# Kernel tuning notes

Hardware: AMD Instinct MI355X
Metric: run time of the kernel (lower is better)

The kernel has to match this reference:

```python
import jax, jax.numpy as jnp
import numpy as np

B, T, D, H = 2, 2048, 1024, 16
HD = D // H  # 64


def setup_inputs() -> dict:
    key = jax.random.key(0)
    ks = jax.random.split(key, 9)
    w = lambda k, shp: (jax.random.normal(k, shp, jnp.float32) * 0.02)
    return {
        "x": jax.random.normal(ks[0], (B, T, D), jnp.float32),
        "Wq": w(ks[1], (D, D)), "bq": jnp.zeros((D,), jnp.float32),
        "Wk": w(ks[2], (D, D)), "bk": jnp.zeros((D,), jnp.float32),
        "Wv": w(ks[3], (D, D)), "bv": jnp.zeros((D,), jnp.float32),
        "Wo": w(ks[4], (D, D)), "bo": jnp.zeros((D,), jnp.float32),
        "Wqs": w(ks[5], (3, HD)), "bqs": jnp.zeros((3,), jnp.float32),
        "Wks": w(ks[6], (3, HD)), "bks": jnp.zeros((3,), jnp.float32),
        "Wvs": w(ks[7], (3, HD)), "bvs": jnp.zeros((3,), jnp.float32),
        "temp": jnp.float32(1.0),
    }


def reference(x, Wq, bq, Wk, bk, Wv, bv, Wo, bo, Wqs, bqs, Wks, bks, Wvs, bvs, temp):
    Bx, Tx, Dx = x.shape
    # project and split heads: [B,H,T,HD]
    split = lambda y: y.reshape(Bx, Tx, H, HD).transpose(0, 2, 1, 3)
    q = split(x @ Wq.T + bq)
    k = split(x @ Wk.T + bk)
    v = split(x @ Wv.T + bv)
    # STP projections to 3-d: [B,H,T,3]
    q_stp = q @ Wqs.T + bqs
    k3 = k @ Wks.T + bks
    v3 = v @ Wvs.T + bvs
    # cross-product term (note: original's layernormed k_sub/v_sub are dead code)
    cross_kv = jnp.cross(k3, v3, axis=-1)  # [B,H,T,3]
    scores = (jnp.einsum('bhqd,bhkd->bhqk', q, k)
              + jnp.einsum('bhqc,bhkc->bhqk', q_stp, cross_kv)) * temp
    attn = jax.nn.softmax(scores, axis=-1)
    out = jnp.einsum('bhqk,bhkd->bhqd', attn, v)  # [B,H,T,HD]
    out = out.transpose(0, 2, 1, 3).reshape(Bx, Tx, Dx)
    return out @ Wo.T + bo
```

## Files before the change

kernel.cpp:

```cpp
#include <hip/hip_runtime.h>
#include <stdint.h>

typedef unsigned short u16;
typedef unsigned int u32;
typedef __attribute__((ext_vector_type(8))) short bf16x8;
typedef __attribute__((ext_vector_type(4))) float f32x4;

__device__ __forceinline__ u16 f2b(float f) {
    union { float f; u32 u; } t; t.f = f;
    return (u16)((t.u + 0x7FFFu + ((t.u >> 16) & 1u)) >> 16);
}
__device__ __forceinline__ u32 pack2(float a, float b) {
    return (u32)f2b(a) | ((u32)f2b(b) << 16);
}
__device__ __forceinline__ u32 cvtpk2(float lo, float hi) {
    u32 r;
    asm("v_cvt_pk_bf16_f32 %0, %1, %2" : "=v"(r) : "v"(lo), "v"(hi));
    return r;
}

__device__ __forceinline__ void async_cp16(const u16* g, const u16* lds_base) {
    __builtin_amdgcn_global_load_lds(
        (const __attribute__((address_space(1))) void*)(uintptr_t)g,
        (__attribute__((address_space(3))) void*)(u32)(uintptr_t)lds_base,
        16, 0, 0);
}

__global__ void cast_all_kernel(const float* __restrict__ x,
                                const float* __restrict__ Wq, const float* __restrict__ Wk,
                                const float* __restrict__ Wv, const float* __restrict__ Wo,
                                u16* __restrict__ xb, u16* __restrict__ Wqb, u16* __restrict__ Wkb,
                                u16* __restrict__ Wvb, u16* __restrict__ Wob) {
    int i = blockIdx.x * blockDim.x + threadIdx.x;
    const float* s; u16* d; int off;
    if (i < 1048576) { s = x; d = xb; off = i; }
    else {
        int j = i - 1048576;
        int w = j >> 18; off = j & 262143;
        if (w == 0) { s = Wq; d = Wqb; }
        else if (w == 1) { s = Wk; d = Wkb; }
        else if (w == 2) { s = Wv; d = Wvb; }
        else { s = Wo; d = Wob; }
    }
    float4 f = ((const float4*)s)[off];
    ((uint2*)d)[off] = make_uint2(pack2(f.x, f.y), pack2(f.z, f.w));
}

__global__ __launch_bounds__(256) void gemm_qkv_kernel(
    const u16* __restrict__ xb,
    const u16* __restrict__ Wq, const u16* __restrict__ Wk, const u16* __restrict__ Wv,
    const float* __restrict__ bq, const float* __restrict__ bk, const float* __restrict__ bv,
    const float* __restrict__ Wqs, const float* __restrict__ bqs,
    const float* __restrict__ Wks, const float* __restrict__ bks,
    const float* __restrict__ Wvs, const float* __restrict__ bvs,
    const float* __restrict__ temp_p,
    u16* __restrict__ qe, u16* __restrict__ ke, u16* __restrict__ vT,
    float4* __restrict__ k3b, float4* __restrict__ v3b)
{
    __shared__ __align__(16) u16 As[2 * 64 * 32];
    __shared__ __align__(16) u16 Bs[2 * 128 * 32];
    const int tid = threadIdx.x;
    const int lane = tid & 63, w = tid >> 6;
    const int wm = w >> 1, wn = w & 1;
    const int l15 = lane & 15, quad = lane >> 4;
    const int M0 = blockIdx.y * 64, N0 = blockIdx.x * 128;
    const int bz = blockIdx.z;

    const u16* W = (bz == 0) ? Wq : (bz == 1) ? Wk : Wv;
    const float* bias = (bz == 0) ? bq : (bz == 1) ? bk : bv;
    const float* Wst = (bz == 0) ? Wqs : (bz == 1) ? Wks : Wvs;
    const float* bst = (bz == 0) ? bqs : (bz == 1) ? bks : bvs;

    f32x4 acc[2][4];
#pragma unroll
    for (int i = 0; i < 2; i++)
#pragma unroll
        for (int j = 0; j < 4; j++) acc[i][j] = (f32x4){0.f, 0.f, 0.f, 0.f};

    int ra = tid >> 2, ca = ((tid & 3) ^ (ra & 3)) * 8;
    const u16* Aga = xb + (size_t)(M0 + ra) * 1024 + ca;
    const u16* Bg0 = W + (size_t)(N0 + ra) * 1024 + ca;
    const u16* Bg1 = W + (size_t)(N0 + ra + 64) * 1024 + ca;
    const int aoff = (w * 64) * 8;
    const int boff0 = (w * 64) * 8;
    const int boff1 = (256 + w * 64) * 8;

    async_cp16(Aga, As + aoff);
    async_cp16(Bg0, Bs + boff0);
    async_cp16(Bg1, Bs + boff1);
    __syncthreads();

    for (int k0 = 0; k0 < 1024; k0 += 32) {
        const int buf = (k0 >> 5) & 1;
        const u16* Asr = As + buf * 2048;
        const u16* Bsr = Bs + buf * 4096;
        if (k0 + 32 < 1024) {
            const int nb_ = buf ^ 1;
            async_cp16(Aga + k0 + 32, As + nb_ * 2048 + aoff);
            async_cp16(Bg0 + k0 + 32, Bs + nb_ * 4096 + boff0);
            async_cp16(Bg1 + k0 + 32, Bs + nb_ * 4096 + boff1);
        }

        bf16x8 af[2], bf[4];
#pragma unroll
        for (int mi = 0; mi < 2; mi++)
            af[mi] = *(const bf16x8*)(Asr + (wm * 32 + mi * 16 + l15) * 32 + ((quad ^ (l15 & 3)) * 8));
#pragma unroll
        for (int ni = 0; ni < 4; ni++)
            bf[ni] = *(const bf16x8*)(Bsr + (wn * 64 + ni * 16 + l15) * 32 + ((quad ^ (l15 & 3)) * 8));
#pragma unroll
        for (int mi = 0; mi < 2; mi++)
#pragma unroll
            for (int ni = 0; ni < 4; ni++)
                acc[mi][ni] = __builtin_amdgcn_mfma_f32_16x16x32_bf16(af[mi], bf[ni], acc[mi][ni], 0, 0, 0);

        __syncthreads();
    }

    const float tau = temp_p[0] * 1.44269504088896f;
    const int nb = N0 + wn * 64;
    const int h = nb >> 6;
    float bias_v[4], wst_v[3][4];
#pragma unroll
    for (int ni = 0; ni < 4; ni++) {
        bias_v[ni] = bias[nb + ni * 16 + l15];
#pragma unroll
        for (int c = 0; c < 3; c++) wst_v[c][ni] = Wst[c * 64 + ni * 16 + l15];
    }
    const float bst0 = bst[0], bst1 = bst[1], bst2 = bst[2];

#pragma unroll
    for (int mi = 0; mi < 2; mi++) {
        int m0 = M0 + wm * 32 + mi * 16 + quad * 4;
        int b = m0 >> 11, t0 = m0 & 2047;
        float p0[4], p1[4], p2[4];
#pragma unroll
        for (int r = 0; r < 4; r++) {
            float a0 = 0.f, a1 = 0.f, a2 = 0.f;
#pragma unroll
            for (int ni = 0; ni < 4; ni++) {
                float v = acc[mi][ni][r] + bias_v[ni];
                a0 += v * wst_v[0][ni];
                a1 += v * wst_v[1][ni];
                a2 += v * wst_v[2][ni];
            }
#pragma unroll
            for (int off = 1; off < 16; off <<= 1) {
                a0 += __shfl_xor(a0, off);
                a1 += __shfl_xor(a1, off);
                a2 += __shfl_xor(a2, off);
            }
            p0[r] = a0 + bst0; p1[r] = a1 + bst1; p2[r] = a2 + bst2;
        }

        if (bz == 0) {
#pragma unroll
            for (int r = 0; r < 4; r++) {
                size_t row = (size_t)((b * 16 + h) * 2048 + (t0 + r));
                u16* qer = qe + row * 96;
#pragma unroll
                for (int ni = 0; ni < 4; ni++)
                    qer[ni * 16 + l15] = f2b((acc[mi][ni][r] + bias_v[ni]) * tau);
                if (l15 == 0) {
                    *(u32*)(qer + 64) = pack2(p0[r] * tau, p1[r] * tau);
                    *(u32*)(qer + 66) = (u32)f2b(p2[r] * tau);
                    uint2 z = make_uint2(0u, 0u);
#pragma unroll
                    for (int j = 68; j < 96; j += 4) *(uint2*)(qer + j) = z;
                }
            }
        } else if (bz == 1) {
#pragma unroll
            for (int r = 0; r < 4; r++) {
                size_t row = (size_t)((b * 16 + h) * 2048 + (t0 + r));
                u16* ker = ke + row * 96;
#pragma unroll
                for (int ni = 0; ni < 4; ni++)
                    ker[ni * 16 + l15] = f2b(acc[mi][ni][r] + bias_v[ni]);
                if (l15 == 0)
                    k3b[row] = make_float4(p0[r], p1[r], p2[r], 0.f);
            }
        } else {
#pragma unroll
            for (int ni = 0; ni < 4; ni++) {
                int hd = ni * 16 + l15;
                float v0 = acc[mi][ni][0] + bias_v[ni];
                float v1 = acc[mi][ni][1] + bias_v[ni];
                float v2 = acc[mi][ni][2] + bias_v[ni];
                float v3 = acc[mi][ni][3] + bias_v[ni];
                *(uint2*)(vT + ((size_t)((b * 16 + h) * 64 + hd)) * 2048 + t0) =
                    make_uint2(pack2(v0, v1), pack2(v2, v3));
            }
            if (l15 == 0) {
#pragma unroll
                for (int r = 0; r < 4; r++) {
                    size_t row = (size_t)((b * 16 + h) * 2048 + (t0 + r));
                    v3b[row] = make_float4(p0[r], p1[r], p2[r], 0.f);
                }
            }
        }
    }
}

__global__ void finish_ext_kernel(const float4* __restrict__ k3b, const float4* __restrict__ v3b,
                                  u16* __restrict__ ke)
{
    int row = blockIdx.x * blockDim.x + threadIdx.x;
    if (row >= 2 * 16 * 2048) return;
    float4 k3 = k3b[row];
    float4 v3 = v3b[row];
    float c0 = k3.y * v3.z - k3.z * v3.y;
    float c1 = k3.z * v3.x - k3.x * v3.z;
    float c2 = k3.x * v3.y - k3.y * v3.x;
    u16* ker = ke + (size_t)row * 96;
    *(u32*)(ker + 64) = pack2(c0, c1);
    *(u32*)(ker + 66) = (u32)f2b(c2);
    uint2 z = make_uint2(0u, 0u);
#pragma unroll
    for (int j = 68; j < 96; j += 4) *(uint2*)(ker + j) = z;
}

__global__ __launch_bounds__(256) void gemm_out_kernel(
    const u16* __restrict__ ao, const u16* __restrict__ Wo, const float* __restrict__ bo,
    float* __restrict__ out)
{
    __shared__ __align__(16) u16 As[2 * 64 * 32];
    __shared__ __align__(16) u16 Bs[2 * 128 * 32];
    const int tid = threadIdx.x;
    const int lane = tid & 63, w = tid >> 6;
    const int wm = w >> 1, wn = w & 1;
    const int l15 = lane & 15, quad = lane >> 4;
    const int M0 = blockIdx.y * 64, N0 = blockIdx.x * 128;

    f32x4 acc[2][4];
#pragma unroll
    for (int i = 0; i < 2; i++)
#pragma unroll
        for (int j = 0; j < 4; j++) acc[i][j] = (f32x4){0.f, 0.f, 0.f, 0.f};

    int ra = tid >> 2, ca = ((tid & 3) ^ (ra & 3)) * 8;
    const u16* Aga = ao + (size_t)(M0 + ra) * 1024 + ca;
    const u16* Bg0 = Wo + (size_t)(N0 + ra) * 1024 + ca;
    const u16* Bg1 = Wo + (size_t)(N0 + ra + 64) * 1024 + ca;
    const int aoff = (w * 64) * 8;
    const int boff0 = (w * 64) * 8;
    const int boff1 = (256 + w * 64) * 8;

    async_cp16(Aga, As + aoff);
    async_cp16(Bg0, Bs + boff0);
    async_cp16(Bg1, Bs + boff1);
    __syncthreads();

    for (int k0 = 0; k0 < 1024; k0 += 32) {
        const int buf = (k0 >> 5) & 1;
        const u16* Asr = As + buf * 2048;
        const u16* Bsr = Bs + buf * 4096;
        if (k0 + 32 < 1024) {
            const int nb_ = buf ^ 1;
            async_cp16(Aga + k0 + 32, As + nb_ * 2048 + aoff);
            async_cp16(Bg0 + k0 + 32, Bs + nb_ * 4096 + boff0);
            async_cp16(Bg1 + k0 + 32, Bs + nb_ * 4096 + boff1);
        }

        bf16x8 af[2], bf[4];
#pragma unroll
        for (int mi = 0; mi < 2; mi++)
            af[mi] = *(const bf16x8*)(Asr + (wm * 32 + mi * 16 + l15) * 32 + ((quad ^ (l15 & 3)) * 8));
#pragma unroll
        for (int ni = 0; ni < 4; ni++)
            bf[ni] = *(const bf16x8*)(Bsr + (wn * 64 + ni * 16 + l15) * 32 + ((quad ^ (l15 & 3)) * 8));
#pragma unroll
        for (int mi = 0; mi < 2; mi++)
#pragma unroll
            for (int ni = 0; ni < 4; ni++)
                acc[mi][ni] = __builtin_amdgcn_mfma_f32_16x16x32_bf16(af[mi], bf[ni], acc[mi][ni], 0, 0, 0);

        __syncthreads();
    }

#pragma unroll
    for (int mi = 0; mi < 2; mi++)
#pragma unroll
        for (int ni = 0; ni < 4; ni++) {
            int n = N0 + wn * 64 + ni * 16 + l15;
            float bias_n = bo[n];
            int m0 = M0 + wm * 32 + mi * 16 + quad * 4;
#pragma unroll
            for (int r = 0; r < 4; r++)
                out[(size_t)(m0 + r) * 1024 + n] = acc[mi][ni][r] + bias_n;
        }
}

__global__ __launch_bounds__(256, 2) void attn_kernel(
    const u16* __restrict__ qe, const u16* __restrict__ ke, const u16* __restrict__ vT,
    u16* __restrict__ out)
{
    __shared__ __align__(16) u16 smem[32768];
    u16* const KsA = smem;
    u16* const VtA = smem + 16384;
    u16* const PsB = smem + 24576;

    const int tid = threadIdx.x;
    const int lane = tid & 63, w = tid >> 6;
    const int kw = w & 1, qw = w >> 1;
    const int l15 = lane & 15, quad = lane >> 4;
    const int lsw = l15 & 7;
    const int bh = blockIdx.y;
    const int q0 = blockIdx.x * 128;

    const u16* qeb = qe + (size_t)bh * 2048 * 96;
    const u16* keb = ke + (size_t)bh * 2048 * 96;
    const u16* vTb = vT + (size_t)bh * 64 * 2048;

    size_t koff[4];
#pragma unroll
    for (int j = 0; j < 4; j++) {
        int r = w * 16 + j * 4 + (lane >> 4);
        koff[j] = (size_t)r * 96 + (size_t)((((lane & 15) ^ (r & 7)) * 8));
    }
    size_t voff[2];
#pragma unroll
    for (int j = 0; j < 2; j++) {
        int r = w * 16 + j * 8 + (lane >> 3);
        voff[j] = (size_t)r * 2048 + (size_t)((((lane & 7) ^ (r & 7)) * 8));
    }

#pragma unroll
    for (int j = 0; j < 4; j++) async_cp16(keb + koff[j], KsA + w * 2048 + j * 512);
#pragma unroll
    for (int j = 0; j < 2; j++) async_cp16(vTb + voff[j], VtA + w * 1024 + j * 512);

    bf16x8 bq[4][3];
#pragma unroll
    for (int s = 0; s < 4; s++) {
        const u16* qrow = qeb + (size_t)(q0 + qw * 64 + s * 16 + l15) * 96;
#pragma unroll
        for (int ks = 0; ks < 3; ks++) bq[s][ks] = *(const bf16x8*)(qrow + ks * 32 + quad * 8);
    }

    f32x4 O[4][4];
    float l_part[4];
#pragma unroll
    for (int s = 0; s < 4; s++) {
        l_part[s] = 0.f;
#pragma unroll
        for (int dt = 0; dt < 4; dt++) O[s][dt] = (f32x4){0.f, 0.f, 0.f, 0.f};
    }

    u16* Pw[4];
#pragma unroll
    for (int s = 0; s < 4; s++) Pw[s] = PsB + (size_t)(qw * 64 + s * 16 + l15) * 64;

    __syncthreads();

    for (int kb = 0; kb < 2048; kb += 64) {
        const int buf = (kb >> 6) & 1;
        const u16* Ks = KsA + buf * 8192;
        const u16* Vt = VtA + buf * 4096;

        if (kb + 64 < 2048) {
            u16* Ksn = KsA + (buf ^ 1) * 8192;
            u16* Vtn = VtA + (buf ^ 1) * 4096;
            const size_t kb96 = (size_t)(kb + 64) * 96;
#pragma unroll
            for (int j = 0; j < 4; j++) async_cp16(keb + kb96 + koff[j], Ksn + w * 2048 + j * 512);
#pragma unroll
            for (int j = 0; j < 2; j++) async_cp16(vTb + (size_t)(kb + 64) + voff[j], Vtn + w * 1024 + j * 512);
        }

        f32x4 S[4][2];
#pragma unroll
        for (int s = 0; s < 4; s++)
#pragma unroll
            for (int nt = 0; nt < 2; nt++) S[s][nt] = (f32x4){0.f, 0.f, 0.f, 0.f};

        __builtin_amdgcn_s_setprio(1);
#pragma unroll
        for (int ks = 0; ks < 3; ks++) {
            bf16x8 ak[2];
#pragma unroll
            for (int nt = 0; nt < 2; nt++)
                ak[nt] = *(const bf16x8*)(Ks + (kw * 32 + nt * 16 + l15) * 128 + (((ks * 4 + quad) ^ lsw) & 15) * 8);
#pragma unroll
            for (int s = 0; s < 4; s++)
#pragma unroll
                for (int nt = 0; nt < 2; nt++)
                    S[s][nt] = __builtin_amdgcn_mfma_f32_16x16x32_bf16(ak[nt], bq[s][ks], S[s][nt], 0, 0, 0);
        }
        __builtin_amdgcn_s_setprio(0);

#pragma unroll
        for (int s = 0; s < 4; s++) {
            float sum = 0.f;
#pragma unroll
            for (int nt = 0; nt < 2; nt++)
#pragma unroll
                for (int r = 0; r < 4; r++) {
                    float p = __builtin_amdgcn_exp2f(S[s][nt][r]);
                    S[s][nt][r] = p;
                    sum += p;
                }
            l_part[s] += sum;
#pragma unroll
            for (int nt = 0; nt < 2; nt++) {
                int c = (kw * 4 + nt * 2 + (quad >> 1)) ^ lsw;
                *(uint2*)(Pw[s] + c * 8 + (quad & 1) * 4) =
                    make_uint2(cvtpk2(S[s][nt][0], S[s][nt][1]), cvtpk2(S[s][nt][2], S[s][nt][3]));
            }
        }

        {
            bf16x8 av[4];
#pragma unroll
            for (int dt = 0; dt < 4; dt++)
                av[dt] = *(const bf16x8*)(Vt + (dt * 16 + l15) * 64 + (((kw * 4 + quad) ^ lsw) & 7) * 8);
            __builtin_amdgcn_s_setprio(1);
#pragma unroll
            for (int s = 0; s < 4; s++) {
                bf16x8 pb = *(const bf16x8*)(Pw[s] + (((kw * 4 + quad) ^ lsw) & 7) * 8);
#pragma unroll
                for (int dt = 0; dt < 4; dt++)
                    O[s][dt] = __builtin_amdgcn_mfma_f32_16x16x32_bf16(av[dt], pb, O[s][dt], 0, 0, 0);
            }
            __builtin_amdgcn_s_setprio(0);
        }

        __syncthreads();
    }

    float* const Ored = (float*)smem;
    float* const Lr = (float*)(smem + 20480);
    if (kw == 1) {
#pragma unroll
        for (int s = 0; s < 4; s++) {
            float l = l_part[s];
            l += __shfl_xor(l, 16);
            l += __shfl_xor(l, 32);
            if (lane < 16) Lr[qw * 64 + s * 16 + l15] = l;
            int qrow = qw * 64 + s * 16 + l15;
#pragma unroll
            for (int dt = 0; dt < 4; dt++) {
                int dc = dt ^ (l15 & 3);
                *(float4*)(Ored + qrow * 68 + dc * 16 + quad * 4) =
                    make_float4(O[s][dt][0], O[s][dt][1], O[s][dt][2], O[s][dt][3]);
            }
        }
    }
    __syncthreads();
    if (kw == 0) {
        const int b = bh >> 4, h = bh & 15;
#pragma unroll
        for (int s = 0; s < 4; s++) {
            float l = l_part[s];
            l += __shfl_xor(l, 16);
            l += __shfl_xor(l, 32);
            int qrow = qw * 64 + s * 16 + l15;
            l += Lr[qrow];
            float linv = 1.0f / l;
            int tq = q0 + qrow;
#pragma unroll
            for (int dt = 0; dt < 4; dt++) {
                int dc = dt ^ (l15 & 3);
                float4 o2 = *(const float4*)(Ored + qrow * 68 + dc * 16 + quad * 4);
                int d = h * 64 + dt * 16 + quad * 4;
                *(uint2*)(out + (size_t)(b * 2048 + tq) * 1024 + d) =
                    make_uint2(cvtpk2((O[s][dt][0] + o2.x) * linv, (O[s][dt][1] + o2.y) * linv),
                               cvtpk2((O[s][dt][2] + o2.z) * linv, (O[s][dt][3] + o2.w) * linv));
            }
        }
    }
}

extern "C" void kernel_launch(void* const* d_in, const int* in_sizes, int n_in,
                              void* d_out, int out_size, void* d_ws, size_t ws_size,
                              hipStream_t stream)
{
    (void)in_sizes; (void)n_in; (void)out_size; (void)ws_size;
    const float* x   = (const float*)d_in[0];
    const float* Wq  = (const float*)d_in[1];
    const float* bq  = (const float*)d_in[2];
    const float* Wk  = (const float*)d_in[3];
    const float* bk  = (const float*)d_in[4];
    const float* Wv  = (const float*)d_in[5];
    const float* bv  = (const float*)d_in[6];
    const float* Wo  = (const float*)d_in[7];
    const float* bo  = (const float*)d_in[8];
    const float* Wqs = (const float*)d_in[9];
    const float* bqs = (const float*)d_in[10];
    const float* Wks = (const float*)d_in[11];
    const float* bks = (const float*)d_in[12];
    const float* Wvs = (const float*)d_in[13];
    const float* bvs = (const float*)d_in[14];
    const float* temp = (const float*)d_in[15];

    char* ws = (char*)d_ws;
    u16* xb  = (u16*)(ws);
    u16* Wqb = (u16*)(ws + 8388608);
    u16* Wkb = (u16*)(ws + 10485760);
    u16* Wvb = (u16*)(ws + 12582912);
    u16* Wob = (u16*)(ws + 14680064);
    u16* qeb = (u16*)(ws + 16777216);
    u16* keb = (u16*)(ws + 29360128);
    u16* vTb = (u16*)(ws + 41943040);
    float4* k3b = (float4*)(ws + 50331648);
    float4* v3b = (float4*)(ws + 51380224);
    u16* aob = (u16*)(ws + 52428800);

    cast_all_kernel<<<8192, 256, 0, stream>>>(x, Wq, Wk, Wv, Wo, xb, Wqb, Wkb, Wvb, Wob);
    gemm_qkv_kernel<<<dim3(8, 64, 3), 256, 0, stream>>>(
        xb, Wqb, Wkb, Wvb, bq, bk, bv, Wqs, bqs, Wks, bks, Wvs, bvs, temp,
        qeb, keb, vTb, k3b, v3b);
    finish_ext_kernel<<<256, 256, 0, stream>>>(k3b, v3b, keb);
    attn_kernel<<<dim3(16, 32), 256, 0, stream>>>(qeb, keb, vTb, aob);
    gemm_out_kernel<<<dim3(8, 64), 256, 0, stream>>>(aob, Wob, bo, (float*)d_out);
}
```

Before: 224.5 us.

## Keep softmax probabilities in registers via permlane swaps instead of LDS round-trip

Converts the exponentiated score tile into the PV MFMA operand layout with v_permlane32_swap and v_permlane16_swap, instead of writing P to shared memory and reading it back. This removes the P LDS buffer, shrinking shared memory from 64KB to 48KB, and raises the launch-bounds occupancy hint from 2 to 3 blocks. The epilogue reduction buffer offset is moved to fit the smaller allocation. The risks are that the lane permutation must exactly match the MFMA B-operand layout, and that the higher occupancy target may limit registers and cause spills.

```diff
diff --git a/kernel.cpp b/kernel.cpp
--- a/kernel.cpp
+++ b/kernel.cpp
@@ -17,6 +17,12 @@
     u32 r;
     asm("v_cvt_pk_bf16_f32 %0, %1, %2" : "=v"(r) : "v"(lo), "v"(hi));
     return r;
+}
+__device__ __forceinline__ void permlane32_swap(u32& a, u32& b) {
+    asm("v_permlane32_swap_b32 %0, %1" : "+v"(a), "+v"(b));
+}
+__device__ __forceinline__ void permlane16_swap(u32& a, u32& b) {
+    asm("v_permlane16_swap_b32 %0, %1" : "+v"(a), "+v"(b));
 }
 
 __device__ __forceinline__ void async_cp16(const u16* g, const u16* lds_base) {
@@ -291,14 +297,13 @@
         }
 }
 
-__global__ __launch_bounds__(256, 2) void attn_kernel(
+__global__ __launch_bounds__(256, 3) void attn_kernel(
     const u16* __restrict__ qe, const u16* __restrict__ ke, const u16* __restrict__ vT,
     u16* __restrict__ out)
 {
-    __shared__ __align__(16) u16 smem[32768];
+    __shared__ __align__(16) u16 smem[24576];
     u16* const KsA = smem;
     u16* const VtA = smem + 16384;
-    u16* const PsB = smem + 24576;
 
     const int tid = threadIdx.x;
     const int lane = tid & 63, w = tid >> 6;
@@ -347,10 +352,6 @@
         for (int dt = 0; dt < 4; dt++) O[s][dt] = (f32x4){0.f, 0.f, 0.f, 0.f};
     }
 
-    u16* Pw[4];
-#pragma unroll
-    for (int s = 0; s < 4; s++) Pw[s] = PsB + (size_t)(qw * 64 + s * 16 + l15) * 64;
-
     __syncthreads();
 
     for (int kb = 0; kb < 2048; kb += 64) {
@@ -389,6 +390,7 @@
         }
         __builtin_amdgcn_s_setprio(0);
 
+        u32 pbw[4][4];
 #pragma unroll
         for (int s = 0; s < 4; s++) {
             float sum = 0.f;
@@ -401,12 +403,15 @@
                     sum += p;
                 }
             l_part[s] += sum;
-#pragma unroll
-            for (int nt = 0; nt < 2; nt++) {
-                int c = (kw * 4 + nt * 2 + (quad >> 1)) ^ lsw;
-                *(uint2*)(Pw[s] + c * 8 + (quad & 1) * 4) =
-                    make_uint2(cvtpk2(S[s][nt][0], S[s][nt][1]), cvtpk2(S[s][nt][2], S[s][nt][3]));
-            }
+            u32 a0 = cvtpk2(S[s][0][0], S[s][0][1]);
+            u32 b0 = cvtpk2(S[s][1][0], S[s][1][1]);
+            u32 a1 = cvtpk2(S[s][0][2], S[s][0][3]);
+            u32 b1 = cvtpk2(S[s][1][2], S[s][1][3]);
+            permlane32_swap(a0, b0);
+            permlane32_swap(a1, b1);
+            permlane16_swap(a0, b0);
+            permlane16_swap(a1, b1);
+            pbw[s][0] = a0; pbw[s][1] = a1; pbw[s][2] = b0; pbw[s][3] = b1;
         }
 
         {
@@ -417,10 +422,12 @@
             __builtin_amdgcn_s_setprio(1);
 #pragma unroll
             for (int s = 0; s < 4; s++) {
-                bf16x8 pb = *(const bf16x8*)(Pw[s] + (((kw * 4 + quad) ^ lsw) & 7) * 8);
+                union { u32 u[4]; bf16x8 v; } pu;
+                pu.u[0] = pbw[s][0]; pu.u[1] = pbw[s][1];
+                pu.u[2] = pbw[s][2]; pu.u[3] = pbw[s][3];
 #pragma unroll
                 for (int dt = 0; dt < 4; dt++)
-                    O[s][dt] = __builtin_amdgcn_mfma_f32_16x16x32_bf16(av[dt], pb, O[s][dt], 0, 0, 0);
+                    O[s][dt] = __builtin_amdgcn_mfma_f32_16x16x32_bf16(av[dt], pu.v, O[s][dt], 0, 0, 0);
             }
             __builtin_amdgcn_s_setprio(0);
         }
@@ -429,7 +436,7 @@
     }
 
     float* const Ored = (float*)smem;
-    float* const Lr = (float*)(smem + 20480);
+    float* const Lr = (float*)(smem + 17664);
     if (kw == 1) {
 #pragma unroll
         for (int s = 0; s < 4; s++) {
```

New measurement: 259.2 us. 1.15x slower.
